# Optimization experiments

Hardware: AMD Instinct MI355X
Metric: run time of the kernel (lower is better)

The kernel has to match this reference:

```python
import jax, jax.numpy as jnp
import numpy as np

B, N, D, H_IMG, W_IMG = 1, 6, 128, 28, 60
HB, WB = 50, 50
HEADS, DH = 4, 32
INNER = HEADS * DH  # 128 == D
Q = HB * WB
NK = N * H_IMG * W_IMG


def _ln(x, w, b, eps=1e-5):
    m = jnp.mean(x, axis=-1, keepdims=True)
    v = jnp.var(x, axis=-1, keepdims=True)
    return (x - m) * jax.lax.rsqrt(v + eps) * w + b


def setup_inputs() -> dict:
    key = jax.random.key(0)
    ks = jax.random.split(key, 20)
    s = 0.02
    inp = {
        "q": jax.random.normal(ks[0], (B, D, HB, WB), jnp.float32),
        "k": jax.random.normal(ks[1], (B, N, D, H_IMG, W_IMG), jnp.float32),
        "v": jax.random.normal(ks[2], (B, N, D, H_IMG, W_IMG), jnp.float32),
        "W_logits": jax.random.uniform(ks[3], (B, Q, NK), jnp.float32),
        "vis_flat": jax.random.randint(ks[4], (B, Q, NK), 0, 2).astype(jnp.int32),
        "skip": jax.random.normal(ks[5], (B, D, HB, WB), jnp.float32),
        # LayerNorm params
        "qn_w": jnp.ones((D,), jnp.float32), "qn_b": jnp.zeros((D,), jnp.float32),
        "kn_w": jnp.ones((D,), jnp.float32), "kn_b": jnp.zeros((D,), jnp.float32),
        "vn_w": jnp.ones((D,), jnp.float32), "vn_b": jnp.zeros((D,), jnp.float32),
        "pre_w": jnp.ones((D,), jnp.float32), "pre_b": jnp.zeros((D,), jnp.float32),
        "post_w": jnp.ones((D,), jnp.float32), "post_b": jnp.zeros((D,), jnp.float32),
        # Linear params, stored [in, out]
        "wq": jax.random.normal(ks[6], (D, INNER), jnp.float32) * s,
        "bq": jnp.zeros((INNER,), jnp.float32),
        "wk": jax.random.normal(ks[7], (D, INNER), jnp.float32) * s,
        "bk": jnp.zeros((INNER,), jnp.float32),
        "wv": jax.random.normal(ks[8], (D, INNER), jnp.float32) * s,
        "bv": jnp.zeros((INNER,), jnp.float32),
        "wp": jax.random.normal(ks[9], (INNER, D), jnp.float32) * s,
        "bp": jnp.zeros((D,), jnp.float32),
        "w1": jax.random.normal(ks[10], (D, 2 * D), jnp.float32) * s,
        "b1": jnp.zeros((2 * D,), jnp.float32),
        "w2": jax.random.normal(ks[11], (2 * D, D), jnp.float32) * s,
        "b2": jnp.zeros((D,), jnp.float32),
    }
    return inp


def reference(q, k, v, W_logits, vis_flat, skip,
              qn_w, qn_b, kn_w, kn_b, vn_w, vn_b, pre_w, pre_b, post_w, post_b,
              wq, bq, wk, bk, wv, bv, wp, bp, w1, b1, w2, b2):
    b, d, Hb, Wb = q.shape
    _, n, _, hi, wi = k.shape
    Qn = Hb * Wb
    # b d H W -> b (H W) d ; b n d h w -> b (n h w) d
    qf = q.reshape(b, d, Qn).transpose(0, 2, 1)
    kf = k.transpose(0, 1, 3, 4, 2).reshape(b, n * hi * wi, d)
    vf = v.transpose(0, 1, 3, 4, 2).reshape(b, n * hi * wi, d)
    qf = _ln(qf, qn_w, qn_b)
    kf = _ln(kf, kn_w, kn_b)
    vf = _ln(vf, vn_w, vn_b)
    qh = (qf @ wq + bq).reshape(b, Qn, HEADS, DH).transpose(0, 2, 1, 3)
    kh = (kf @ wk + bk).reshape(b, -1, HEADS, DH).transpose(0, 2, 1, 3)
    vh = (vf @ wv + bv).reshape(b, -1, HEADS, DH).transpose(0, 2, 1, 3)
    scale = DH ** (-0.5)
    logits = jnp.einsum('bhqd,bhkd->bhqk', qh, kh) * scale  # [b,h,Q,NK]
    neg_inf = jnp.finfo(logits.dtype).min
    logits = jnp.where(vis_flat[:, None] == 0, neg_inf, logits)
    logits = logits * W_logits[:, None]  # multiplicative EAF weighting
    attn = jax.nn.softmax(logits, axis=-1)
    out = jnp.einsum('bhqk,bhkd->bhqd', attn, vh)
    out = out.transpose(0, 2, 1, 3).reshape(b, Qn, INNER)
    out = out @ wp + bp
    z = out + skip.reshape(b, d, Qn).transpose(0, 2, 1)
    z = _ln(z, pre_w, pre_b)
    z = z + (jax.nn.gelu(z @ w1 + b1, approximate=False) @ w2 + b2)
    z = _ln(z, post_w, post_b)
    return z.transpose(0, 2, 1).reshape(b, d, Hb, Wb)
```

## Files before the change

kernel.cpp:

```cpp
#include <hip/hip_runtime.h>
#include <hip/hip_bf16.h>
#include <math.h>

typedef short short8 __attribute__((ext_vector_type(8)));
typedef float floatx4 __attribute__((ext_vector_type(4)));

#define D 128
#define Q 2500
#define QPAD 2560
#define NK 10080
#define NKPAD 10112
#define SPLITS 35
#define CPS 9
#define QSCALE 0.25501268426834347f
#define NEGBIG -3.0e38f

__device__ __forceinline__ unsigned short f2bf(float f) {
    unsigned u = __float_as_uint(f);
    unsigned r = (u + 0x7fffu + ((u >> 16) & 1u)) >> 16;
    return (unsigned short)r;
}
__device__ __forceinline__ unsigned pack2bf(float lo, float hi) {
    unsigned u0 = __float_as_uint(lo) + 0x8000u;
    unsigned u1 = __float_as_uint(hi) + 0x8000u;
    return (u0 >> 16) | (u1 & 0xffff0000u);
}
__device__ __forceinline__ float bflo(unsigned u) { return __uint_as_float(u << 16); }
__device__ __forceinline__ float bfhi(unsigned u) { return __uint_as_float(u & 0xffff0000u); }

__global__ void wcvt_kernel(const float* __restrict__ wq, const float* __restrict__ wk,
                            const float* __restrict__ wv, const float* __restrict__ wp,
                            const float* __restrict__ w1, const float* __restrict__ w2,
                            unsigned short* __restrict__ wqT, unsigned short* __restrict__ wkT,
                            unsigned short* __restrict__ wvT, unsigned short* __restrict__ wpT,
                            unsigned short* __restrict__ w1T, unsigned short* __restrict__ w2T) {
    int idx = blockIdx.x * 256 + threadIdx.x;
    if (idx < 49152) {
        int m = idx >> 14;
        int local = idx & 16383;
        int n = local >> 7, kk = local & 127;
        const float* w = (m == 0) ? wq : ((m == 1) ? wk : wv);
        unsigned short* o = (m == 0) ? wqT : ((m == 1) ? wkT : wvT);
        o[local] = f2bf(w[kk * 128 + n]);
    } else if (idx < 65536) {
        int local = idx - 49152;
        int n = local >> 7, kk = local & 127;
        int b = kk >> 5, j = kk & 31;
        int ko = b * 32 + ((j & 1) ? 16 + (j >> 1) : (j >> 1));
        wpT[local] = f2bf(wp[ko * 128 + n]);
    } else if (idx < 98304) {
        int local = idx - 65536;
        int n = local >> 7, kk = local & 127;
        w1T[local] = f2bf(w1[kk * 256 + n]);
    } else {
        int local = idx - 98304;
        int n = local >> 8, kk = local & 255;
        w2T[local] = f2bf(w2[kk * 128 + n]);
    }
}

__global__ __launch_bounds__(256) void ln_kernel(
    const float* __restrict__ qi, const float* __restrict__ ki, const float* __restrict__ vi,
    const float* __restrict__ qw, const float* __restrict__ qb,
    const float* __restrict__ kw, const float* __restrict__ kb,
    const float* __restrict__ vw, const float* __restrict__ vb,
    unsigned short* __restrict__ xq, unsigned short* __restrict__ xk,
    unsigned short* __restrict__ xv) {
    __shared__ float lds[16 * 132];
    int bid = blockIdx.x, t = threadIdx.x;
    const float* src; unsigned short* dst; const float *g, *b;
    int S, valid;
    if (bid < 157) {
        int p0 = bid * 16;
        src = qi + p0; S = Q; dst = xq + p0 * D; g = qw; b = qb;
        valid = Q - p0; if (valid > 16) valid = 16;
    } else if (bid < 787) {
        int tt = bid - 157;
        int n = tt / 105, r = (tt - n * 105) * 16;
        src = ki + (size_t)(n * 128) * 1680 + r; S = 1680;
        dst = xk + (n * 1680 + r) * D; g = kw; b = kb; valid = 16;
    } else {
        int tt = bid - 787;
        int n = tt / 105, r = (tt - n * 105) * 16;
        src = vi + (size_t)(n * 128) * 1680 + r; S = 1680;
        dst = xv + (n * 1680 + r) * D; g = vw; b = vb; valid = 16;
    }
    int c4 = t & 3, d = t >> 2;
    floatx4 fa = {0.f, 0.f, 0.f, 0.f}, fb = {0.f, 0.f, 0.f, 0.f};
    if (c4 * 4 < valid) {
        fa = *(const floatx4*)(src + d * S + c4 * 4);
        fb = *(const floatx4*)(src + (d + 64) * S + c4 * 4);
    }
    #pragma unroll
    for (int j = 0; j < 4; j++) {
        lds[(c4 * 4 + j) * 132 + d] = fa[j];
        lds[(c4 * 4 + j) * 132 + d + 64] = fb[j];
    }
    __syncthreads();
    int lane = t & 63, wv = t >> 6;
    int pos = wv * 4 + (lane >> 4), l15 = lane & 15;
    floatx4 xa = *(const floatx4*)(&lds[pos * 132 + l15 * 8]);
    floatx4 xb = *(const floatx4*)(&lds[pos * 132 + l15 * 8 + 4]);
    float s = 0.f, ss = 0.f;
    #pragma unroll
    for (int j = 0; j < 4; j++) { s += xa[j] + xb[j]; ss += xa[j] * xa[j] + xb[j] * xb[j]; }
    #pragma unroll
    for (int m = 1; m <= 8; m <<= 1) { s += __shfl_xor(s, m, 64); ss += __shfl_xor(ss, m, 64); }
    float mean = s * (1.0f / 128.0f);
    float var = ss * (1.0f / 128.0f) - mean * mean;
    float rstd = rsqrtf(var + 1e-5f);
    floatx4 g0 = *(const floatx4*)(g + l15 * 8), g1 = *(const floatx4*)(g + l15 * 8 + 4);
    floatx4 b0 = *(const floatx4*)(b + l15 * 8), b1 = *(const floatx4*)(b + l15 * 8 + 4);
    short8 o;
    #pragma unroll
    for (int j = 0; j < 4; j++) {
        o[j] = (short)f2bf((xa[j] - mean) * rstd * g0[j] + b0[j]);
        o[4 + j] = (short)f2bf((xb[j] - mean) * rstd * g1[j] + b1[j]);
    }
    if (pos < valid) *(short8*)(dst + pos * D + l15 * 8) = o;
}

__global__ __launch_bounds__(256) void proj_kernel(
    const unsigned short* __restrict__ xq, const unsigned short* __restrict__ xk,
    const unsigned short* __restrict__ xv,
    const unsigned short* __restrict__ wqT, const unsigned short* __restrict__ wkT,
    const unsigned short* __restrict__ wvT,
    const float* __restrict__ bq, const float* __restrict__ bk, const float* __restrict__ bv,
    unsigned short* __restrict__ qh, unsigned short* __restrict__ kh,
    unsigned short* __restrict__ vhT) {
    __shared__ short vlds[128 * 72];
    int bid = blockIdx.x;
    const unsigned short *src, *wT; const float* bias; int mb, mode; float scale;
    if (bid < 40)       { mode = 0; src = xq; wT = wqT; bias = bq; mb = bid * 64; scale = QSCALE; }
    else if (bid < 198) { mode = 1; src = xk; wT = wkT; bias = bk; mb = (bid - 40) * 64; scale = 1.0f; }
    else                { mode = 2; src = xv; wT = wvT; bias = bv; mb = (bid - 198) * 64; scale = 1.0f; }
    int t = threadIdx.x, wave = t >> 6, lane = t & 63;
    int l15 = lane & 15, quad = lane >> 4;
    int m0 = mb + wave * 16;
    floatx4 acc[8];
    #pragma unroll
    for (int i = 0; i < 8; i++) acc[i] = (floatx4){0.f, 0.f, 0.f, 0.f};
    #pragma unroll
    for (int kf = 0; kf < 4; kf++) {
        short8 A = *(const short8*)(src + (m0 + l15) * D + kf * 32 + quad * 8);
        #pragma unroll
        for (int nt = 0; nt < 8; nt++) {
            short8 Bv = *(const short8*)(wT + (nt * 16 + l15) * D + kf * 32 + quad * 8);
            acc[nt] = __builtin_amdgcn_mfma_f32_16x16x32_bf16(A, Bv, acc[nt], 0, 0, 0);
        }
    }
    if (mode != 2) {
        unsigned short* dst = (mode == 0) ? qh : kh;
        #pragma unroll
        for (int nt = 0; nt < 8; nt++) {
            float bb = bias[nt * 16 + l15];
            #pragma unroll
            for (int r = 0; r < 4; r++)
                dst[(m0 + quad * 4 + r) * D + nt * 16 + l15] = f2bf((acc[nt][r] + bb) * scale);
        }
    } else {
        #pragma unroll
        for (int nt = 0; nt < 8; nt++) {
            float bb = bias[nt * 16 + l15];
            #pragma unroll
            for (int r = 0; r < 4; r++)
                vlds[(nt * 16 + l15) * 72 + (wave * 16 + quad * 4 + r)] =
                    (short)f2bf(acc[nt][r] + bb);
        }
        __syncthreads();
        int pr = t & 31, dd = t >> 5;
        int sub = pr >> 4, i = pr & 15;
        #pragma unroll
        for (int pass = 0; pass < 16; pass++) {
            int d = pass * 8 + dd;
            unsigned lo = (unsigned short)vlds[d * 72 + sub * 32 + i];
            unsigned hi = (unsigned short)vlds[d * 72 + sub * 32 + 16 + i];
            *(unsigned*)(vhT + (size_t)d * NKPAD + mb + sub * 32 + 2 * i) = lo | (hi << 16);
        }
    }
}

__global__ __launch_bounds__(256) void attn_kernel(
    const unsigned short* __restrict__ qh, const unsigned short* __restrict__ kh,
    const unsigned short* __restrict__ vhT,
    const float* __restrict__ Wl, const int* __restrict__ vis,
    unsigned* __restrict__ OpartU, float* __restrict__ lpart) {
    __shared__ unsigned pP[4 * 4 * 16 * 20];
    int bid = blockIdx.x;
    int split = bid % SPLITS, qt = bid / SPLITS;
    int t = threadIdx.x, wave = t >> 6, lane = t & 63;
    int l15 = lane & 15, quad = lane >> 4;
    int qb = qt * 64 + wave * 16;
    int k00 = split * (CPS * 32);
    unsigned* pw = pP + wave * 1280;

    short8 qA[4];
    #pragma unroll
    for (int h = 0; h < 4; h++)
        qA[h] = *(const short8*)(qh + (qb + l15) * D + h * 32 + quad * 8);

    const float* wrow[4]; const int* vrow[4];
    #pragma unroll
    for (int r = 0; r < 4; r++) {
        int row = qb + quad * 4 + r;
        row = row < Q ? row : (Q - 1);
        wrow[r] = Wl + (size_t)row * NK;
        vrow[r] = vis + (size_t)row * NK;
    }

    const floatx4 zf = {0.f, 0.f, 0.f, 0.f};
    floatx4 O[4][2];
    float lacc[4][4];
    #pragma unroll
    for (int h = 0; h < 4; h++) {
        O[h][0] = zf; O[h][1] = zf;
        #pragma unroll
        for (int r = 0; r < 4; r++) lacc[h][r] = 0.f;
    }

    #pragma unroll 1
    for (int c = 0; c < CPS; c++) {
        int k0 = k00 + c * 32;
        float w0[4], w1[4]; int msk0[4], msk1[4];
        #pragma unroll
        for (int r = 0; r < 4; r++) {
            w0[r] = wrow[r][k0 + l15];
            w1[r] = wrow[r][k0 + 16 + l15];
            msk0[r] = vrow[r][k0 + l15];
            msk1[r] = vrow[r][k0 + 16 + l15];
        }
        #pragma unroll
        for (int h = 0; h < 4; h++) {
            short8 kB0 = *(const short8*)(kh + (k0 + l15) * D + h * 32 + quad * 8);
            short8 kB1 = *(const short8*)(kh + (k0 + 16 + l15) * D + h * 32 + quad * 8);
            floatx4 S0 = __builtin_amdgcn_mfma_f32_16x16x32_bf16(qA[h], kB0, zf, 0, 0, 0);
            floatx4 S1 = __builtin_amdgcn_mfma_f32_16x16x32_bf16(qA[h], kB1, zf, 0, 0, 0);
            #pragma unroll
            for (int r = 0; r < 4; r++) {
                float L0 = (msk0[r] ? S0[r] : NEGBIG) * w0[r];
                float L1 = (msk1[r] ? S1[r] : NEGBIG) * w1[r];
                float p0 = exp2f(L0), p1 = exp2f(L1);
                lacc[h][r] += p0 + p1;
                pw[h * 320 + (quad * 4 + r) * 20 + l15] = pack2bf(p0, p1);
            }
        }
        #pragma unroll
        for (int h = 0; h < 4; h++) {
            short8 P = *(const short8*)(pw + h * 320 + l15 * 20 + quad * 4);
            short8 vB0 = *(const short8*)(vhT + (size_t)(h * 32 + l15) * NKPAD + k0 + quad * 8);
            short8 vB1 = *(const short8*)(vhT + (size_t)(h * 32 + 16 + l15) * NKPAD + k0 + quad * 8);
            O[h][0] = __builtin_amdgcn_mfma_f32_16x16x32_bf16(P, vB0, O[h][0], 0, 0, 0);
            O[h][1] = __builtin_amdgcn_mfma_f32_16x16x32_bf16(P, vB1, O[h][1], 0, 0, 0);
        }
    }

    #pragma unroll
    for (int h = 0; h < 4; h++)
        #pragma unroll
        for (int r = 0; r < 4; r++) {
            float lv = lacc[h][r];
            lv += __shfl_xor(lv, 1, 64);
            lv += __shfl_xor(lv, 2, 64);
            lv += __shfl_xor(lv, 4, 64);
            lv += __shfl_xor(lv, 8, 64);
            int row = qb + quad * 4 + r;
            int base = (split * QPAD + row) * 4 + h;
            if (l15 == 0) lpart[base] = lv;
            OpartU[base * 16 + l15] = pack2bf(O[h][0][r], O[h][1][r]);
        }
}

__global__ void linv_kernel(const float* __restrict__ lpart, float* __restrict__ linv) {
    int i = blockIdx.x * 256 + threadIdx.x;
    float s = 0.f;
    #pragma unroll 1
    for (int sp = 0; sp < SPLITS; sp++) s += lpart[sp * QPAD * 4 + i];
    linv[i] = 1.0f / fmaxf(s, 1e-30f);
}

__global__ void combine_kernel(const unsigned* __restrict__ OpartU,
                               const float* __restrict__ linv,
                               unsigned* __restrict__ A1u) {
    int idx = blockIdx.x * 256 + threadIdx.x;
    float lo = 0.f, hi = 0.f;
    #pragma unroll 1
    for (int sp = 0; sp < SPLITS; sp++) {
        unsigned u = OpartU[(size_t)sp * (QPAD * 64) + idx];
        lo += bflo(u);
        hi += bfhi(u);
    }
    int q = idx >> 6, t6 = idx & 63;
    float inv = linv[q * 4 + (t6 >> 4)];
    A1u[idx] = pack2bf(lo * inv, hi * inv);
}

__global__ __launch_bounds__(256) void mlp_kernel(
    const unsigned short* __restrict__ A1s, const unsigned short* __restrict__ wpT,
    const float* __restrict__ bp, const float* __restrict__ skip,
    const float* __restrict__ pre_w, const float* __restrict__ pre_b,
    const unsigned short* __restrict__ w1T, const float* __restrict__ b1,
    const unsigned short* __restrict__ w2T, const float* __restrict__ b2,
    const float* __restrict__ post_w, const float* __restrict__ post_b,
    float* __restrict__ out) {
    __shared__ __align__(16) char smem[51200];
    short* Z1 = (short*)smem;
    short* H1 = (short*)(smem + 17408);
    float* Zout = (float*)smem;

    int qb = blockIdx.x * 64;
    int t = threadIdx.x, wave = t >> 6, lane = t & 63;
    int l15 = lane & 15, quad = lane >> 4;
    int m0 = wave * 16;

    floatx4 z[8];
    #pragma unroll
    for (int i = 0; i < 8; i++) z[i] = (floatx4){0.f, 0.f, 0.f, 0.f};
    #pragma unroll
    for (int kf = 0; kf < 4; kf++) {
        short8 A = *(const short8*)(A1s + (qb + m0 + l15) * D + kf * 32 + quad * 8);
        #pragma unroll
        for (int nt = 0; nt < 8; nt++) {
            short8 Bv = *(const short8*)(wpT + (nt * 16 + l15) * D + kf * 32 + quad * 8);
            z[nt] = __builtin_amdgcn_mfma_f32_16x16x32_bf16(A, Bv, z[nt], 0, 0, 0);
        }
    }
    float Zv[8][4];
    #pragma unroll
    for (int nt = 0; nt < 8; nt++) {
        int n = nt * 16 + l15;
        float bb = bp[n];
        #pragma unroll
        for (int r = 0; r < 4; r++) {
            int q = qb + m0 + quad * 4 + r;
            int qc = q < Q ? q : (Q - 1);
            Zv[nt][r] = z[nt][r] + bb + skip[n * Q + qc];
        }
    }
    float Zn[8][4];
    {
        #pragma unroll
        for (int r = 0; r < 4; r++) {
            float s1 = 0.f, s2 = 0.f;
            #pragma unroll
            for (int nt = 0; nt < 8; nt++) { s1 += Zv[nt][r]; s2 += Zv[nt][r] * Zv[nt][r]; }
            #pragma unroll
            for (int m = 1; m <= 8; m <<= 1) { s1 += __shfl_xor(s1, m, 64); s2 += __shfl_xor(s2, m, 64); }
            float mean = s1 * (1.0f / 128.0f);
            float var = s2 * (1.0f / 128.0f) - mean * mean;
            float rstd = rsqrtf(var + 1e-5f);
            #pragma unroll
            for (int nt = 0; nt < 8; nt++) Zn[nt][r] = (Zv[nt][r] - mean) * rstd;
        }
        #pragma unroll
        for (int nt = 0; nt < 8; nt++) {
            int n = nt * 16 + l15;
            float g = pre_w[n], be = pre_b[n];
            #pragma unroll
            for (int r = 0; r < 4; r++) {
                Zn[nt][r] = Zn[nt][r] * g + be;
                Z1[(m0 + quad * 4 + r) * 136 + n] = (short)f2bf(Zn[nt][r]);
            }
        }
    }
    {
        floatx4 h2[16];
        #pragma unroll
        for (int i = 0; i < 16; i++) h2[i] = (floatx4){0.f, 0.f, 0.f, 0.f};
        #pragma unroll
        for (int kf = 0; kf < 4; kf++) {
            short8 A = *(const short8*)(Z1 + (m0 + l15) * 136 + kf * 32 + quad * 8);
            #pragma unroll
            for (int nt = 0; nt < 16; nt++) {
                short8 Bv = *(const short8*)(w1T + (nt * 16 + l15) * D + kf * 32 + quad * 8);
                h2[nt] = __builtin_amdgcn_mfma_f32_16x16x32_bf16(A, Bv, h2[nt], 0, 0, 0);
            }
        }
        #pragma unroll
        for (int nt = 0; nt < 16; nt++) {
            int n = nt * 16 + l15;
            float bb = b1[n];
            #pragma unroll
            for (int r = 0; r < 4; r++) {
                float x = h2[nt][r] + bb;
                float gl = 0.5f * x * (1.0f + erff(x * 0.70710678118654752f));
                H1[(m0 + quad * 4 + r) * 264 + n] = (short)f2bf(gl);
            }
        }
    }
    floatx4 o3[8];
    #pragma unroll
    for (int i = 0; i < 8; i++) o3[i] = (floatx4){0.f, 0.f, 0.f, 0.f};
    #pragma unroll
    for (int kf = 0; kf < 8; kf++) {
        short8 A = *(const short8*)(H1 + (m0 + l15) * 264 + kf * 32 + quad * 8);
        #pragma unroll
        for (int nt = 0; nt < 8; nt++) {
            short8 Bv = *(const short8*)(w2T + (nt * 16 + l15) * 256 + kf * 32 + quad * 8);
            o3[nt] = __builtin_amdgcn_mfma_f32_16x16x32_bf16(A, Bv, o3[nt], 0, 0, 0);
        }
    }
    float Z2[8][4];
    #pragma unroll
    for (int nt = 0; nt < 8; nt++) {
        int n = nt * 16 + l15;
        float bb = b2[n];
        #pragma unroll
        for (int r = 0; r < 4; r++) Z2[nt][r] = Zn[nt][r] + o3[nt][r] + bb;
    }
    float Zo[8][4];
    {
        #pragma unroll
        for (int r = 0; r < 4; r++) {
            float s1 = 0.f, s2 = 0.f;
            #pragma unroll
            for (int nt = 0; nt < 8; nt++) { s1 += Z2[nt][r]; s2 += Z2[nt][r] * Z2[nt][r]; }
            #pragma unroll
            for (int m = 1; m <= 8; m <<= 1) { s1 += __shfl_xor(s1, m, 64); s2 += __shfl_xor(s2, m, 64); }
            float mean = s1 * (1.0f / 128.0f);
            float var = s2 * (1.0f / 128.0f) - mean * mean;
            float rstd = rsqrtf(var + 1e-5f);
            #pragma unroll
            for (int nt = 0; nt < 8; nt++) Zo[nt][r] = (Z2[nt][r] - mean) * rstd;
        }
        #pragma unroll
        for (int nt = 0; nt < 8; nt++) {
            int n = nt * 16 + l15;
            float g = post_w[n], be = post_b[n];
            #pragma unroll
            for (int r = 0; r < 4; r++) Zo[nt][r] = Zo[nt][r] * g + be;
        }
    }
    __syncthreads();
    #pragma unroll
    for (int nt = 0; nt < 8; nt++)
        #pragma unroll
        for (int r = 0; r < 4; r++)
            Zout[(nt * 16 + l15) * 65 + m0 + quad * 4 + r] = Zo[nt][r];
    __syncthreads();
    {
        int pl = t & 63;
        int q = qb + pl;
        if (q < Q) {
            #pragma unroll
            for (int it = 0; it < 32; it++) {
                int n = it * 4 + (t >> 6);
                out[n * Q + q] = Zout[n * 65 + pl];
            }
        }
    }
}

extern "C" void kernel_launch(void* const* d_in, const int* in_sizes, int n_in,
                              void* d_out, int out_size, void* d_ws, size_t ws_size,
                              hipStream_t stream) {
    (void)in_sizes; (void)n_in; (void)out_size; (void)ws_size;
    const float* q      = (const float*)d_in[0];
    const float* k      = (const float*)d_in[1];
    const float* v      = (const float*)d_in[2];
    const float* Wl     = (const float*)d_in[3];
    const int*   vis    = (const int*)  d_in[4];
    const float* skip   = (const float*)d_in[5];
    const float* qn_w   = (const float*)d_in[6];
    const float* qn_b   = (const float*)d_in[7];
    const float* kn_w   = (const float*)d_in[8];
    const float* kn_b   = (const float*)d_in[9];
    const float* vn_w   = (const float*)d_in[10];
    const float* vn_b   = (const float*)d_in[11];
    const float* pre_w  = (const float*)d_in[12];
    const float* pre_b  = (const float*)d_in[13];
    const float* post_w = (const float*)d_in[14];
    const float* post_b = (const float*)d_in[15];
    const float* wq     = (const float*)d_in[16];
    const float* bq     = (const float*)d_in[17];
    const float* wk     = (const float*)d_in[18];
    const float* bk     = (const float*)d_in[19];
    const float* wv     = (const float*)d_in[20];
    const float* bv     = (const float*)d_in[21];
    const float* wp     = (const float*)d_in[22];
    const float* bp     = (const float*)d_in[23];
    const float* w1     = (const float*)d_in[24];
    const float* b1     = (const float*)d_in[25];
    const float* w2     = (const float*)d_in[26];
    const float* b2     = (const float*)d_in[27];
    float* out = (float*)d_out;

    char* ws = (char*)d_ws;
    unsigned short* xq  = (unsigned short*)(ws + 0);
    unsigned short* xk  = (unsigned short*)(ws + 655360);
    unsigned short* xv  = (unsigned short*)(ws + 3244032);
    unsigned short* qh  = (unsigned short*)(ws + 5832704);
    unsigned short* kh  = (unsigned short*)(ws + 6488064);
    unsigned short* vhT = (unsigned short*)(ws + 9076736);
    unsigned short* wqT = (unsigned short*)(ws + 11665408);
    unsigned short* wkT = (unsigned short*)(ws + 11698176);
    unsigned short* wvT = (unsigned short*)(ws + 11730944);
    unsigned short* wpT = (unsigned short*)(ws + 11763712);
    unsigned short* w1T = (unsigned short*)(ws + 11796480);
    unsigned short* w2T = (unsigned short*)(ws + 11862016);
    unsigned* OpartU    = (unsigned*)(ws + 11927552);
    float* lpart        = (float*)(ws + 34865152);
    float* linv         = (float*)(ws + 36298752);
    unsigned* A1u       = (unsigned*)(ws + 36339712);

    wcvt_kernel<<<dim3(512), dim3(256), 0, stream>>>(wq, wk, wv, wp, w1, w2,
                                                     wqT, wkT, wvT, wpT, w1T, w2T);
    ln_kernel<<<dim3(1417), dim3(256), 0, stream>>>(q, k, v, qn_w, qn_b, kn_w, kn_b, vn_w, vn_b,
                                                    xq, xk, xv);
    proj_kernel<<<dim3(356), dim3(256), 0, stream>>>(xq, xk, xv, wqT, wkT, wvT, bq, bk, bv,
                                                     qh, kh, vhT);
    attn_kernel<<<dim3(40 * SPLITS), dim3(256), 0, stream>>>(qh, kh, vhT, Wl, vis, OpartU, lpart);
    linv_kernel<<<dim3(40), dim3(256), 0, stream>>>(lpart, linv);
    combine_kernel<<<dim3(640), dim3(256), 0, stream>>>(OpartU, linv, A1u);
    mlp_kernel<<<dim3(40), dim3(256), 0, stream>>>((const unsigned short*)A1u, wpT, bp, skip,
                                                   pre_w, pre_b, w1T, b1, w2T, b2,
                                                   post_w, post_b, out);
}
```

Before: 426.1 us.

## Vectorize and prefetch W/vis loads via LDS double buffer; vectorize combine

The attention kernel now loads W_logits and vis with coalesced 16-byte vector loads one chunk ahead. It packs them into bf16 with the mask in the sign bit and stages them in a double-buffered LDS tile, replacing strided scalar global loads. The mask-and-multiply is folded into a single FMA before exp2. The combine kernel processes four words per thread with uint4 loads, and the split buffers are re-strided to a tighter pitch. This costs extra LDS traffic and rounds W to bf16, which changes precision.

```diff
diff --git a/kernel.cpp b/kernel.cpp
--- a/kernel.cpp
+++ b/kernel.cpp
@@ -12,6 +12,8 @@
 #define NKPAD 10112
 #define SPLITS 35
 #define CPS 9
+#define OPS 163920
+#define LPS 10308
 #define QSCALE 0.25501268426834347f
 #define NEGBIG -3.0e38f
 
@@ -27,6 +29,11 @@
 }
 __device__ __forceinline__ float bflo(unsigned u) { return __uint_as_float(u << 16); }
 __device__ __forceinline__ float bfhi(unsigned u) { return __uint_as_float(u & 0xffff0000u); }
+__device__ __forceinline__ unsigned packwv(float w, int v) {
+    unsigned b = __float_as_uint(w);
+    unsigned r = (b + 0x7fffu + ((b >> 16) & 1u)) >> 16;
+    return v ? r : (r | 0x8000u);
+}
 
 __global__ void wcvt_kernel(const float* __restrict__ wq, const float* __restrict__ wk,
                             const float* __restrict__ wv, const float* __restrict__ wp,
@@ -186,6 +193,7 @@
     const float* __restrict__ Wl, const int* __restrict__ vis,
     unsigned* __restrict__ OpartU, float* __restrict__ lpart) {
     __shared__ unsigned pP[4 * 4 * 16 * 20];
+    __shared__ unsigned wbuf[4 * 2 * 16 * 16];
     int bid = blockIdx.x;
     int split = bid % SPLITS, qt = bid / SPLITS;
     int t = threadIdx.x, wave = t >> 6, lane = t & 63;
@@ -193,20 +201,21 @@
     int qb = qt * 64 + wave * 16;
     int k00 = split * (CPS * 32);
     unsigned* pw = pP + wave * 1280;
+    unsigned* wb = wbuf + wave * 512;
+    unsigned short* wbs = (unsigned short*)wb;
 
     short8 qA[4];
     #pragma unroll
     for (int h = 0; h < 4; h++)
-        qA[h] = *(const short8*)(qh + (qb + l15) * D + h * 32 + quad * 8);
-
-    const float* wrow[4]; const int* vrow[4];
-    #pragma unroll
-    for (int r = 0; r < 4; r++) {
-        int row = qb + quad * 4 + r;
-        row = row < Q ? row : (Q - 1);
-        wrow[r] = Wl + (size_t)row * NK;
-        vrow[r] = vis + (size_t)row * NK;
-    }
+        qA[h] = *(const short8*)(qh + (size_t)(qb + l15) * D + h * 32 + quad * 8);
+
+    int lr = lane >> 3, lc = lane & 7;
+    int row0 = qb + lr;      row0 = row0 < Q ? row0 : Q - 1;
+    int row1 = qb + 8 + lr;  row1 = row1 < Q ? row1 : Q - 1;
+    const float* wp0 = Wl + (size_t)row0 * NK + k00 + lc * 4;
+    const float* wp1 = Wl + (size_t)row1 * NK + k00 + lc * 4;
+    const int*  vp0 = vis + (size_t)row0 * NK + k00 + lc * 4;
+    const int*  vp1 = vis + (size_t)row1 * NK + k00 + lc * 4;
 
     const floatx4 zf = {0.f, 0.f, 0.f, 0.f};
     floatx4 O[4][2];
@@ -218,28 +227,49 @@
         for (int r = 0; r < 4; r++) lacc[h][r] = 0.f;
     }
 
-    #pragma unroll 1
+    floatx4 wA0 = *(const floatx4*)(wp0);
+    floatx4 wA1 = *(const floatx4*)(wp1);
+    int4    vA0 = *(const int4*)(vp0);
+    int4    vA1 = *(const int4*)(vp1);
+    {
+        uint2 s0, s1;
+        s0.x = packwv(wA0[0], vA0.x) | (packwv(wA0[1], vA0.y) << 16);
+        s0.y = packwv(wA0[2], vA0.z) | (packwv(wA0[3], vA0.w) << 16);
+        s1.x = packwv(wA1[0], vA1.x) | (packwv(wA1[1], vA1.y) << 16);
+        s1.y = packwv(wA1[2], vA1.z) | (packwv(wA1[3], vA1.w) << 16);
+        *(uint2*)(wb + lr * 16 + lc * 2) = s0;
+        *(uint2*)(wb + (8 + lr) * 16 + lc * 2) = s1;
+    }
+
     for (int c = 0; c < CPS; c++) {
+        int buf = c & 1;
         int k0 = k00 + c * 32;
-        float w0[4], w1[4]; int msk0[4], msk1[4];
-        #pragma unroll
-        for (int r = 0; r < 4; r++) {
-            w0[r] = wrow[r][k0 + l15];
-            w1[r] = wrow[r][k0 + 16 + l15];
-            msk0[r] = vrow[r][k0 + l15];
-            msk1[r] = vrow[r][k0 + 16 + l15];
+        if (c + 1 < CPS) {
+            wA0 = *(const floatx4*)(wp0 + (c + 1) * 32);
+            wA1 = *(const floatx4*)(wp1 + (c + 1) * 32);
+            vA0 = *(const int4*)(vp0 + (c + 1) * 32);
+            vA1 = *(const int4*)(vp1 + (c + 1) * 32);
+        }
+        float a2[8], b2[8];
+        #pragma unroll
+        for (int i = 0; i < 8; i++) {
+            int rr = i >> 1, hf = i & 1;
+            unsigned u = wbs[buf * 512 + (quad * 4 + rr) * 32 + hf * 16 + l15];
+            float wf = __uint_as_float((u & 0x7fffu) << 16);
+            bool msk = (u & 0x8000u) != 0;
+            a2[i] = msk ? 0.f : wf;
+            b2[i] = msk ? wf * NEGBIG : 0.f;
         }
         #pragma unroll
         for (int h = 0; h < 4; h++) {
-            short8 kB0 = *(const short8*)(kh + (k0 + l15) * D + h * 32 + quad * 8);
-            short8 kB1 = *(const short8*)(kh + (k0 + 16 + l15) * D + h * 32 + quad * 8);
+            short8 kB0 = *(const short8*)(kh + (size_t)(k0 + l15) * D + h * 32 + quad * 8);
+            short8 kB1 = *(const short8*)(kh + (size_t)(k0 + 16 + l15) * D + h * 32 + quad * 8);
             floatx4 S0 = __builtin_amdgcn_mfma_f32_16x16x32_bf16(qA[h], kB0, zf, 0, 0, 0);
             floatx4 S1 = __builtin_amdgcn_mfma_f32_16x16x32_bf16(qA[h], kB1, zf, 0, 0, 0);
             #pragma unroll
             for (int r = 0; r < 4; r++) {
-                float L0 = (msk0[r] ? S0[r] : NEGBIG) * w0[r];
-                float L1 = (msk1[r] ? S1[r] : NEGBIG) * w1[r];
-                float p0 = exp2f(L0), p1 = exp2f(L1);
+                float p0 = exp2f(S0[r] * a2[2 * r] + b2[2 * r]);
+                float p1 = exp2f(S1[r] * a2[2 * r + 1] + b2[2 * r + 1]);
                 lacc[h][r] += p0 + p1;
                 pw[h * 320 + (quad * 4 + r) * 20 + l15] = pack2bf(p0, p1);
             }
@@ -251,6 +281,16 @@
             short8 vB1 = *(const short8*)(vhT + (size_t)(h * 32 + 16 + l15) * NKPAD + k0 + quad * 8);
             O[h][0] = __builtin_amdgcn_mfma_f32_16x16x32_bf16(P, vB0, O[h][0], 0, 0, 0);
             O[h][1] = __builtin_amdgcn_mfma_f32_16x16x32_bf16(P, vB1, O[h][1], 0, 0, 0);
+        }
+        if (c + 1 < CPS) {
+            uint2 s0, s1;
+            s0.x = packwv(wA0[0], vA0.x) | (packwv(wA0[1], vA0.y) << 16);
+            s0.y = packwv(wA0[2], vA0.z) | (packwv(wA0[3], vA0.w) << 16);
+            s1.x = packwv(wA1[0], vA1.x) | (packwv(wA1[1], vA1.y) << 16);
+            s1.y = packwv(wA1[2], vA1.z) | (packwv(wA1[3], vA1.w) << 16);
+            int nbuf = (buf ^ 1) * 256;
+            *(uint2*)(wb + nbuf + lr * 16 + lc * 2) = s0;
+            *(uint2*)(wb + nbuf + (8 + lr) * 16 + lc * 2) = s1;
         }
     }
 
@@ -264,34 +304,42 @@
             lv += __shfl_xor(lv, 4, 64);
             lv += __shfl_xor(lv, 8, 64);
             int row = qb + quad * 4 + r;
-            int base = (split * QPAD + row) * 4 + h;
-            if (l15 == 0) lpart[base] = lv;
-            OpartU[base * 16 + l15] = pack2bf(O[h][0][r], O[h][1][r]);
+            if (l15 == 0) lpart[(size_t)split * LPS + row * 4 + h] = lv;
+            OpartU[(size_t)split * OPS + (row * 4 + h) * 16 + l15] =
+                pack2bf(O[h][0][r], O[h][1][r]);
         }
 }
 
 __global__ void linv_kernel(const float* __restrict__ lpart, float* __restrict__ linv) {
     int i = blockIdx.x * 256 + threadIdx.x;
     float s = 0.f;
-    #pragma unroll 1
-    for (int sp = 0; sp < SPLITS; sp++) s += lpart[sp * QPAD * 4 + i];
+    #pragma unroll 7
+    for (int sp = 0; sp < SPLITS; sp++) s += lpart[(size_t)sp * LPS + i];
     linv[i] = 1.0f / fmaxf(s, 1e-30f);
 }
 
 __global__ void combine_kernel(const unsigned* __restrict__ OpartU,
                                const float* __restrict__ linv,
                                unsigned* __restrict__ A1u) {
-    int idx = blockIdx.x * 256 + threadIdx.x;
-    float lo = 0.f, hi = 0.f;
-    #pragma unroll 1
+    int idx = (blockIdx.x * 256 + threadIdx.x) * 4;
+    float lo0 = 0.f, lo1 = 0.f, lo2 = 0.f, lo3 = 0.f;
+    float hi0 = 0.f, hi1 = 0.f, hi2 = 0.f, hi3 = 0.f;
+    #pragma unroll 5
     for (int sp = 0; sp < SPLITS; sp++) {
-        unsigned u = OpartU[(size_t)sp * (QPAD * 64) + idx];
-        lo += bflo(u);
-        hi += bfhi(u);
-    }
-    int q = idx >> 6, t6 = idx & 63;
-    float inv = linv[q * 4 + (t6 >> 4)];
-    A1u[idx] = pack2bf(lo * inv, hi * inv);
+        uint4 u = *(const uint4*)(OpartU + (size_t)sp * OPS + idx);
+        lo0 += bflo(u.x); hi0 += bfhi(u.x);
+        lo1 += bflo(u.y); hi1 += bfhi(u.y);
+        lo2 += bflo(u.z); hi2 += bfhi(u.z);
+        lo3 += bflo(u.w); hi3 += bfhi(u.w);
+    }
+    int q = idx >> 6;
+    float inv = linv[q * 4 + ((idx & 63) >> 4)];
+    uint4 o;
+    o.x = pack2bf(lo0 * inv, hi0 * inv);
+    o.y = pack2bf(lo1 * inv, hi1 * inv);
+    o.z = pack2bf(lo2 * inv, hi2 * inv);
+    o.w = pack2bf(lo3 * inv, hi3 * inv);
+    *(uint4*)(A1u + idx) = o;
 }
 
 __global__ __launch_bounds__(256) void mlp_kernel(
@@ -498,9 +546,9 @@
     unsigned short* w1T = (unsigned short*)(ws + 11796480);
     unsigned short* w2T = (unsigned short*)(ws + 11862016);
     unsigned* OpartU    = (unsigned*)(ws + 11927552);
-    float* lpart        = (float*)(ws + 34865152);
-    float* linv         = (float*)(ws + 36298752);
-    unsigned* A1u       = (unsigned*)(ws + 36339712);
+    float* lpart        = (float*)(ws + 34876352);
+    float* linv         = (float*)(ws + 36319472);
+    unsigned* A1u       = (unsigned*)(ws + 655360);
 
     wcvt_kernel<<<dim3(512), dim3(256), 0, stream>>>(wq, wk, wv, wp, w1, w2,
                                                      wqT, wkT, wvT, wpT, w1T, w2T);
@@ -510,7 +558,7 @@
                                                      qh, kh, vhT);
     attn_kernel<<<dim3(40 * SPLITS), dim3(256), 0, stream>>>(qh, kh, vhT, Wl, vis, OpartU, lpart);
     linv_kernel<<<dim3(40), dim3(256), 0, stream>>>(lpart, linv);
-    combine_kernel<<<dim3(640), dim3(256), 0, stream>>>(OpartU, linv, A1u);
+    combine_kernel<<<dim3(160), dim3(256), 0, stream>>>(OpartU, linv, A1u);
     mlp_kernel<<<dim3(40), dim3(256), 0, stream>>>((const unsigned short*)A1u, wpT, bp, skip,
                                                    pre_w, pre_b, w1T, b1, w2T, b2,
                                                    post_w, post_b, out);
```

Result: faster. 412.0 us (-3.3%).

## Transpose attention MFMAs, shuffle P in registers, vectorize and prefetch mask loads

Applied to the files above, without the earlier changes.

Swaps the MFMA operand order so each lane holds one query row's scores. P is then packed and redistributed with cross-lane shuffles instead of going through shared memory. W_logits and the visibility mask are read as 16-byte vectors and prefetched one chunk ahead. Masking is folded into one FMA per score. Splits drop from 35 to 21, which shrinks the partial-output buffers and the combine work but gives fewer blocks to fill the GPU. The wp permutation, output layout and workspace offsets change to match the new lane mapping.

```diff
diff --git a/kernel.cpp b/kernel.cpp
--- a/kernel.cpp
+++ b/kernel.cpp
@@ -4,14 +4,17 @@
 
 typedef short short8 __attribute__((ext_vector_type(8)));
 typedef float floatx4 __attribute__((ext_vector_type(4)));
+typedef int   intx4  __attribute__((ext_vector_type(4)));
 
 #define D 128
 #define Q 2500
 #define QPAD 2560
 #define NK 10080
 #define NKPAD 10112
-#define SPLITS 35
-#define CPS 9
+#define SPLITS 21
+#define CPS 15
+#define OPS 163904
+#define LPS 10304
 #define QSCALE 0.25501268426834347f
 #define NEGBIG -3.0e38f
 
@@ -45,9 +48,7 @@
     } else if (idx < 65536) {
         int local = idx - 49152;
         int n = local >> 7, kk = local & 127;
-        int b = kk >> 5, j = kk & 31;
-        int ko = b * 32 + ((j & 1) ? 16 + (j >> 1) : (j >> 1));
-        wpT[local] = f2bf(wp[ko * 128 + n]);
+        wpT[local] = f2bf(wp[kk * 128 + n]);
     } else if (idx < 98304) {
         int local = idx - 65536;
         int n = local >> 7, kk = local & 127;
@@ -180,101 +181,114 @@
     }
 }
 
-__global__ __launch_bounds__(256) void attn_kernel(
+__global__ __launch_bounds__(256, 3) void attn_kernel(
     const unsigned short* __restrict__ qh, const unsigned short* __restrict__ kh,
     const unsigned short* __restrict__ vhT,
     const float* __restrict__ Wl, const int* __restrict__ vis,
     unsigned* __restrict__ OpartU, float* __restrict__ lpart) {
-    __shared__ unsigned pP[4 * 4 * 16 * 20];
     int bid = blockIdx.x;
-    int split = bid % SPLITS, qt = bid / SPLITS;
-    int t = threadIdx.x, wave = t >> 6, lane = t & 63;
+    int split = bid % SPLITS, qt4 = bid / SPLITS;
+    int lane = threadIdx.x & 63, wave = threadIdx.x >> 6;
     int l15 = lane & 15, quad = lane >> 4;
-    int qb = qt * 64 + wave * 16;
+    int qb = (qt4 * 4 + wave) * 16;
     int k00 = split * (CPS * 32);
-    unsigned* pw = pP + wave * 1280;
-
-    short8 qA[4];
+
+    short8 qB[4];
     #pragma unroll
     for (int h = 0; h < 4; h++)
-        qA[h] = *(const short8*)(qh + (qb + l15) * D + h * 32 + quad * 8);
-
-    const float* wrow[4]; const int* vrow[4];
-    #pragma unroll
-    for (int r = 0; r < 4; r++) {
-        int row = qb + quad * 4 + r;
-        row = row < Q ? row : (Q - 1);
-        wrow[r] = Wl + (size_t)row * NK;
-        vrow[r] = vis + (size_t)row * NK;
-    }
+        qB[h] = *(const short8*)(qh + (qb + l15) * D + h * 32 + quad * 8);
+
+    int wrow = qb + l15; if (wrow >= Q) wrow = Q - 1;
+    const float* wp = Wl + (size_t)wrow * NK + k00 + quad * 4;
+    const int*   vp = vis + (size_t)wrow * NK + k00 + quad * 4;
 
     const floatx4 zf = {0.f, 0.f, 0.f, 0.f};
     floatx4 O[4][2];
-    float lacc[4][4];
-    #pragma unroll
-    for (int h = 0; h < 4; h++) {
-        O[h][0] = zf; O[h][1] = zf;
-        #pragma unroll
-        for (int r = 0; r < 4; r++) lacc[h][r] = 0.f;
-    }
+    float lacc[4];
+    #pragma unroll
+    for (int h = 0; h < 4; h++) { O[h][0] = zf; O[h][1] = zf; lacc[h] = 0.f; }
+
+    int sidx[4];
+    #pragma unroll
+    for (int jj = 0; jj < 4; jj++)
+        sidx[jj] = l15 + 16 * ((quad & 1) * 2 + (jj >> 1));
+    bool hiTile = quad >= 2;
+
+    floatx4 wc0 = *(const floatx4*)(wp);
+    floatx4 wc1 = *(const floatx4*)(wp + 16);
+    intx4   vc0 = *(const intx4*)(vp);
+    intx4   vc1 = *(const intx4*)(vp + 16);
 
     #pragma unroll 1
     for (int c = 0; c < CPS; c++) {
         int k0 = k00 + c * 32;
-        float w0[4], w1[4]; int msk0[4], msk1[4];
+        floatx4 wn0, wn1; intx4 vn0, vn1;
+        if (c + 1 < CPS) {
+            wn0 = *(const floatx4*)(wp + (c + 1) * 32);
+            wn1 = *(const floatx4*)(wp + (c + 1) * 32 + 16);
+            vn0 = *(const intx4*)(vp + (c + 1) * 32);
+            vn1 = *(const intx4*)(vp + (c + 1) * 32 + 16);
+        }
+        float a2[8], b2[8];
         #pragma unroll
         for (int r = 0; r < 4; r++) {
-            w0[r] = wrow[r][k0 + l15];
-            w1[r] = wrow[r][k0 + 16 + l15];
-            msk0[r] = vrow[r][k0 + l15];
-            msk1[r] = vrow[r][k0 + 16 + l15];
+            a2[r]     = vc0[r] ? wc0[r] : 0.f;
+            b2[r]     = vc0[r] ? 0.f : wc0[r] * NEGBIG;
+            a2[4 + r] = vc1[r] ? wc1[r] : 0.f;
+            b2[4 + r] = vc1[r] ? 0.f : wc1[r] * NEGBIG;
         }
         #pragma unroll
         for (int h = 0; h < 4; h++) {
-            short8 kB0 = *(const short8*)(kh + (k0 + l15) * D + h * 32 + quad * 8);
-            short8 kB1 = *(const short8*)(kh + (k0 + 16 + l15) * D + h * 32 + quad * 8);
-            floatx4 S0 = __builtin_amdgcn_mfma_f32_16x16x32_bf16(qA[h], kB0, zf, 0, 0, 0);
-            floatx4 S1 = __builtin_amdgcn_mfma_f32_16x16x32_bf16(qA[h], kB1, zf, 0, 0, 0);
+            short8 kA0 = *(const short8*)(kh + (k0 + l15) * D + h * 32 + quad * 8);
+            short8 kA1 = *(const short8*)(kh + (k0 + 16 + l15) * D + h * 32 + quad * 8);
+            floatx4 S0 = __builtin_amdgcn_mfma_f32_16x16x32_bf16(kA0, qB[h], zf, 0, 0, 0);
+            floatx4 S1 = __builtin_amdgcn_mfma_f32_16x16x32_bf16(kA1, qB[h], zf, 0, 0, 0);
+            float p0[4], p1[4];
             #pragma unroll
             for (int r = 0; r < 4; r++) {
-                float L0 = (msk0[r] ? S0[r] : NEGBIG) * w0[r];
-                float L1 = (msk1[r] ? S1[r] : NEGBIG) * w1[r];
-                float p0 = exp2f(L0), p1 = exp2f(L1);
-                lacc[h][r] += p0 + p1;
-                pw[h * 320 + (quad * 4 + r) * 20 + l15] = pack2bf(p0, p1);
+                p0[r] = exp2f(S0[r] * a2[r] + b2[r]);
+                p1[r] = exp2f(S1[r] * a2[4 + r] + b2[4 + r]);
+                lacc[h] += p0[r] + p1[r];
             }
-        }
-        #pragma unroll
-        for (int h = 0; h < 4; h++) {
-            short8 P = *(const short8*)(pw + h * 320 + l15 * 20 + quad * 4);
-            short8 vB0 = *(const short8*)(vhT + (size_t)(h * 32 + l15) * NKPAD + k0 + quad * 8);
-            short8 vB1 = *(const short8*)(vhT + (size_t)(h * 32 + 16 + l15) * NKPAD + k0 + quad * 8);
-            O[h][0] = __builtin_amdgcn_mfma_f32_16x16x32_bf16(P, vB0, O[h][0], 0, 0, 0);
-            O[h][1] = __builtin_amdgcn_mfma_f32_16x16x32_bf16(P, vB1, O[h][1], 0, 0, 0);
-        }
-    }
-
-    #pragma unroll
-    for (int h = 0; h < 4; h++)
-        #pragma unroll
-        for (int r = 0; r < 4; r++) {
-            float lv = lacc[h][r];
-            lv += __shfl_xor(lv, 1, 64);
-            lv += __shfl_xor(lv, 2, 64);
-            lv += __shfl_xor(lv, 4, 64);
-            lv += __shfl_xor(lv, 8, 64);
-            int row = qb + quad * 4 + r;
-            int base = (split * QPAD + row) * 4 + h;
-            if (l15 == 0) lpart[base] = lv;
-            OpartU[base * 16 + l15] = pack2bf(O[h][0][r], O[h][1][r]);
-        }
+            unsigned PP0[2] = {pack2bf(p0[0], p0[1]), pack2bf(p0[2], p0[3])};
+            unsigned PP1[2] = {pack2bf(p1[0], p1[1]), pack2bf(p1[2], p1[3])};
+            union { unsigned u[4]; short8 s; } pb;
+            #pragma unroll
+            for (int jj = 0; jj < 4; jj++) {
+                unsigned s0 = (unsigned)__shfl((int)PP0[jj & 1], sidx[jj], 64);
+                unsigned s1 = (unsigned)__shfl((int)PP1[jj & 1], sidx[jj], 64);
+                pb.u[jj] = hiTile ? s1 : s0;
+            }
+            short8 vA0 = *(const short8*)(vhT + (size_t)(h * 32 + l15) * NKPAD + k0 + quad * 8);
+            short8 vA1 = *(const short8*)(vhT + (size_t)(h * 32 + 16 + l15) * NKPAD + k0 + quad * 8);
+            O[h][0] = __builtin_amdgcn_mfma_f32_16x16x32_bf16(vA0, pb.s, O[h][0], 0, 0, 0);
+            O[h][1] = __builtin_amdgcn_mfma_f32_16x16x32_bf16(vA1, pb.s, O[h][1], 0, 0, 0);
+        }
+        wc0 = wn0; wc1 = wn1; vc0 = vn0; vc1 = vn1;
+    }
+
+    int row = qb + l15;
+    #pragma unroll
+    for (int h = 0; h < 4; h++) {
+        float lv = lacc[h];
+        lv += __shfl_xor(lv, 16, 64);
+        lv += __shfl_xor(lv, 32, 64);
+        if (quad == 0) lpart[(size_t)split * LPS + row * 4 + h] = lv;
+        #pragma unroll
+        for (int tl = 0; tl < 2; tl++) {
+            uint2 o2;
+            o2.x = pack2bf(O[h][tl][0], O[h][tl][1]);
+            o2.y = pack2bf(O[h][tl][2], O[h][tl][3]);
+            *(uint2*)(OpartU + (size_t)split * OPS + ((size_t)row * 4 + h) * 16 + tl * 8 + quad * 2) = o2;
+        }
+    }
 }
 
 __global__ void linv_kernel(const float* __restrict__ lpart, float* __restrict__ linv) {
     int i = blockIdx.x * 256 + threadIdx.x;
     float s = 0.f;
-    #pragma unroll 1
-    for (int sp = 0; sp < SPLITS; sp++) s += lpart[sp * QPAD * 4 + i];
+    #pragma unroll
+    for (int sp = 0; sp < SPLITS; sp++) s += lpart[(size_t)sp * LPS + i];
     linv[i] = 1.0f / fmaxf(s, 1e-30f);
 }
 
@@ -283,14 +297,13 @@
                                unsigned* __restrict__ A1u) {
     int idx = blockIdx.x * 256 + threadIdx.x;
     float lo = 0.f, hi = 0.f;
-    #pragma unroll 1
+    #pragma unroll
     for (int sp = 0; sp < SPLITS; sp++) {
-        unsigned u = OpartU[(size_t)sp * (QPAD * 64) + idx];
+        unsigned u = OpartU[(size_t)sp * OPS + idx];
         lo += bflo(u);
         hi += bfhi(u);
     }
-    int q = idx >> 6, t6 = idx & 63;
-    float inv = linv[q * 4 + (t6 >> 4)];
+    float inv = linv[idx >> 4];
     A1u[idx] = pack2bf(lo * inv, hi * inv);
 }
 
@@ -498,9 +511,9 @@
     unsigned short* w1T = (unsigned short*)(ws + 11796480);
     unsigned short* w2T = (unsigned short*)(ws + 11862016);
     unsigned* OpartU    = (unsigned*)(ws + 11927552);
-    float* lpart        = (float*)(ws + 34865152);
-    float* linv         = (float*)(ws + 36298752);
-    unsigned* A1u       = (unsigned*)(ws + 36339712);
+    float* lpart        = (float*)(ws + 25695488);
+    float* linv         = (float*)(ws + 26561024);
+    unsigned* A1u       = (unsigned*)(ws + 655360);
 
     wcvt_kernel<<<dim3(512), dim3(256), 0, stream>>>(wq, wk, wv, wp, w1, w2,
                                                      wqT, wkT, wvT, wpT, w1T, w2T);
```

Result: slower. 446.9 us (+4.9%).
